# Kernel optimization log

Hardware: AMD Instinct MI355X
Metric: run time of the kernel (lower is better)

## Reference

```python
import jax, jax.numpy as jnp
import numpy as np

B, N, D = 2, 2048, 512
H, VD = 8, 64  # v_dim = hid_dim / n_head


def setup_inputs() -> dict:
    key = jax.random.key(0)
    k1, k2, k3, k4 = jax.random.split(key, 4)
    inputs = jax.random.normal(k1, (B, N, D), dtype=jnp.float32)
    # lecun_normal: std = 1/sqrt(fan_in) with fan_in = D
    s = 1.0 / np.sqrt(D)
    q_w = jax.random.normal(k2, (H, D, VD), dtype=jnp.float32) * s
    k_w = jax.random.normal(k3, (H, D, VD), dtype=jnp.float32) * s
    v_w = jax.random.normal(k4, (H, D, VD), dtype=jnp.float32) * s
    return {"inputs": inputs, "q_w": q_w, "k_w": k_w, "v_w": v_w}


def reference(inputs, q_w, k_w, v_w):
    # QKV projections: [B,N,D] x [H,D,VD] -> [B,H,N,VD]
    q = jnp.einsum('bnj,hjk->bhnk', inputs, q_w)
    k = jnp.einsum('bnj,hjk->bhnk', inputs, k_w)
    v = jnp.einsum('bnj,hjk->bhnk', inputs, v_w)
    scale = 1.0 / jnp.sqrt(jnp.asarray(VD, dtype=q.dtype))
    scores = jnp.einsum('bhik,bhjk->bhij', q, k) * scale  # [B,H,N,N]
    att = jax.nn.softmax(scores, axis=-1)
    out = jnp.einsum('bhnj,bhjd->bhnd', att, v)  # [B,H,N,VD]
    out = jnp.transpose(out, (0, 2, 1, 3)).reshape(inputs.shape[0], -1, H * VD)  # [B,N,hid_dim]
    # keras GELU default is exact (non-approximate)
    return jax.nn.gelu(out, approximate=False)
```

## Files before the change

kernel.cpp:

```cpp
#include <hip/hip_runtime.h>
#include <hip/hip_bf16.h>
#include <math.h>

#define BB 2
#define NN 2048
#define DD 512
#define HH 8
#define VD 64

typedef _Float16 half8 __attribute__((ext_vector_type(8)));
typedef _Float16 half4 __attribute__((ext_vector_type(4)));
typedef __fp16 fp16x2 __attribute__((ext_vector_type(2)));
typedef float f32x4 __attribute__((ext_vector_type(4)));

#define GLDS16(gp, lp) __builtin_amdgcn_global_load_lds( \
    (const __attribute__((address_space(1))) void*)(gp), \
    (__attribute__((address_space(3))) void*)(lp), 16, 0, 0)

__device__ __forceinline__ float fexp2(float x) {
#if __has_builtin(__builtin_amdgcn_exp2f)
    return __builtin_amdgcn_exp2f(x);
#else
    return exp2f(x);
#endif
}

__device__ __forceinline__ void stage8(const _Float16* gsrc, size_t ldg, int r0,
                                       _Float16* lbase, int lane) {
    int r8 = lane >> 3;
    int ce = ((lane & 7) ^ r8) << 3;
    const _Float16* g = gsrc + (size_t)(r0 + r8) * ldg + ce;
    GLDS16(g, lbase);
}

__device__ __forceinline__ half8 frag_ld(const _Float16* tile, int row, int cb) {
    int off = row * 128 + (cb ^ ((row & 7) << 4));
    return *(const half8*)((const char*)tile + off);
}

__device__ __forceinline__ float gelu_exact(float v) {
    return 0.5f * v * (1.f + erff(v * 0.70710678118654752f));
}

__global__ __launch_bounds__(256) void prep_kernel(
    const float* __restrict__ x,
    const float* __restrict__ qw, const float* __restrict__ kw,
    const float* __restrict__ vw,
    _Float16* __restrict__ wt, _Float16* __restrict__ xh)
{
    __shared__ float ls[64][65];
    const int t = threadIdx.x;
    const int bid = blockIdx.x;
    if (bid < 192) {
        const int kc = bid & 7, h = (bid >> 3) & 7, ty = bid >> 6;
        const float* src = (ty == 0) ? qw : (ty == 1) ? kw : vw;
#pragma unroll
        for (int j = 0; j < 4; ++j) {
            int idx = t + 256 * j;
            int k = idx >> 4, o4 = idx & 15;
            float4 v = *(const float4*)(src + ((size_t)(h * DD + kc * 64 + k) * VD + o4 * 4));
            ls[k][o4 * 4 + 0] = v.x; ls[k][o4 * 4 + 1] = v.y;
            ls[k][o4 * 4 + 2] = v.z; ls[k][o4 * 4 + 3] = v.w;
        }
        __syncthreads();
#pragma unroll
        for (int j = 0; j < 4; ++j) {
            int idx = t + 256 * j;
            int o = idx >> 4, k4 = idx & 15;
            half4 hv;
#pragma unroll
            for (int i = 0; i < 4; ++i) hv[i] = (_Float16)ls[k4 * 4 + i][o];
            *(half4*)(wt + ((size_t)(ty * HH + h) * VD + o) * DD + kc * 64 + k4 * 4) = hv;
        }
    } else {
        size_t idx = ((size_t)(bid - 192) * 256 + t) * 8;
        float4 a = *(const float4*)(x + idx);
        float4 b = *(const float4*)(x + idx + 4);
        half8 hv;
        hv[0] = (_Float16)a.x; hv[1] = (_Float16)a.y;
        hv[2] = (_Float16)a.z; hv[3] = (_Float16)a.w;
        hv[4] = (_Float16)b.x; hv[5] = (_Float16)b.y;
        hv[6] = (_Float16)b.z; hv[7] = (_Float16)b.w;
        *(half8*)(xh + idx) = hv;
    }
}

__global__ __launch_bounds__(256) void qkv_proj_kernel(
    const _Float16* __restrict__ xh,
    const _Float16* __restrict__ wt,
    _Float16* __restrict__ qsp,
    _Float16* __restrict__ kbp,
    _Float16* __restrict__ vtp)
{
    __shared__ __align__(16) _Float16 xls[2][4096];
    __shared__ __align__(16) _Float16 wls[2][12288];
    const int t = threadIdx.x;
    const int wave = t >> 6, lane = t & 63;
    const int lq = lane & 15, g = lane >> 4;
    const int bid = blockIdx.x;
    const int h = bid & 7;
    const int m0 = (bid >> 3) * 64;
    const int rbase = 32 * (wave >> 1);
    const int cbase = 96 * (wave & 1);

    f32x4 acc[2][6];
#pragma unroll
    for (int a = 0; a < 2; ++a)
#pragma unroll
        for (int c = 0; c < 6; ++c) acc[a][c] = (f32x4){0.f, 0.f, 0.f, 0.f};

    auto stage = [&](int buf, int ks) {
#pragma unroll
        for (int j = 0; j < 2; ++j) {
            int i = wave * 2 + j;
            stage8(xh + (size_t)m0 * DD + ks * 64, DD, i * 8, &xls[buf][i * 512], lane);
        }
#pragma unroll
        for (int j = 0; j < 6; ++j) {
            int i = wave * 6 + j;
            int ty = i >> 3;
            int ol = (i & 7) * 8;
            stage8(wt + ((size_t)(ty * HH + h) * VD + ol) * DD + ks * 64, DD, 0,
                   &wls[buf][i * 512], lane);
        }
    };

    stage(0, 0);
    stage(1, 1);
    for (int ks = 0; ks < 8; ++ks) {
        const int buf = ks & 1;
        if (ks < 7) asm volatile("s_waitcnt vmcnt(8)" ::: "memory");
        else        asm volatile("s_waitcnt vmcnt(0)" ::: "memory");
        __builtin_amdgcn_s_barrier();
        half8 af[2][2];
        half8 bf[6][2];
#pragma unroll
        for (int amt = 0; amt < 2; ++amt) {
            af[amt][0] = frag_ld(xls[buf], rbase + amt * 16 + lq, 16 * g);
            af[amt][1] = frag_ld(xls[buf], rbase + amt * 16 + lq, 64 + 16 * g);
        }
#pragma unroll
        for (int ct = 0; ct < 6; ++ct) {
            int wr = cbase + ct * 16 + lq;
            bf[ct][0] = frag_ld(wls[buf], wr, 16 * g);
            bf[ct][1] = frag_ld(wls[buf], wr, 64 + 16 * g);
        }
        asm volatile("s_waitcnt lgkmcnt(0)" ::: "memory");
        __builtin_amdgcn_sched_barrier(0);
        __builtin_amdgcn_s_barrier();
        if (ks + 2 < 8) stage(buf, ks + 2);
        __builtin_amdgcn_s_setprio(1);
#pragma unroll
        for (int ct = 0; ct < 6; ++ct) {
#pragma unroll
            for (int amt = 0; amt < 2; ++amt) {
                acc[amt][ct] = __builtin_amdgcn_mfma_f32_16x16x32_f16(af[amt][0], bf[ct][0], acc[amt][ct], 0, 0, 0);
                acc[amt][ct] = __builtin_amdgcn_mfma_f32_16x16x32_f16(af[amt][1], bf[ct][1], acc[amt][ct], 0, 0, 0);
            }
        }
        __builtin_amdgcn_s_setprio(0);
    }

#pragma unroll
    for (int ct = 0; ct < 6; ++ct) {
        int gcol = cbase + ct * 16 + lq;
        int ty = gcol >> 6, o = gcol & 63;
#pragma unroll
        for (int amt = 0; amt < 2; ++amt) {
#pragma unroll
            for (int i = 0; i < 4; ++i) {
                int ng = m0 + rbase + amt * 16 + 4 * g + i;
                int b = ng >> 11, nb = ng & (NN - 1);
                size_t bh = (size_t)(b * HH + h);
                float v = acc[amt][ct][i];
                if (ty == 0)      qsp[(bh * NN + nb) * VD + o] = (_Float16)(v * 0.18033688011112042f);
                else if (ty == 1) kbp[(bh * NN + nb) * VD + o] = (_Float16)v;
                else              vtp[(bh * VD + o) * NN + nb] = (_Float16)v;
            }
        }
    }
}

__global__ __launch_bounds__(256) void attn_kernel(
    const _Float16* __restrict__ qs,
    const _Float16* __restrict__ kb,
    const _Float16* __restrict__ vt,
    float* __restrict__ out)
{
    constexpr int NITER = NN / 64;
    __shared__ __align__(16) _Float16 kls[3][4096];
    __shared__ __align__(16) _Float16 vls[3][4096];
    const int t = threadIdx.x;
    const int wave = t >> 6, lane = t & 63;
    const int lq = lane & 15, g = lane >> 4;
    const int bid = blockIdx.x;
    const int xcd = bid & 7;
    const int bh = xcd * 2 + ((bid >> 3) & 1);
    const int qt = bid >> 4;
    const int qbase = qt * 64 + wave * 16;

    half8 qf[2];
    {
        const _Float16* qp = qs + ((size_t)bh * NN + qbase + lq) * VD + 8 * g;
        qf[0] = *(const half8*)qp;
        qf[1] = *(const half8*)(qp + 32);
    }

    const int r8 = lane >> 3;
    const int dchunk = (lane & 7) ^ r8;
    const int krow0 = 16 * (r8 >> 2) + 4 * wave + (r8 & 3);
    const _Float16* kgA = kb + (size_t)bh * NN * VD + (size_t)krow0 * VD + dchunk * 8;
    const int kvst = 16 * (dchunk & 3) + 8 * (dchunk >> 2);
    const _Float16* vgA = vt + (size_t)bh * VD * NN + (size_t)(wave * 16 + r8) * NN + kvst;

    f32x4 oacc[4];
#pragma unroll
    for (int mt = 0; mt < 4; ++mt) oacc[mt] = (f32x4){0.f, 0.f, 0.f, 0.f};
    float lsum = 0.f;

    auto stagekv = [&](_Float16* kd, _Float16* vd, int itn) {
        const _Float16* kp = kgA + (size_t)itn * (64 * VD);
        GLDS16(kp,           kd + wave * 1024);
        GLDS16(kp + 32 * VD, kd + wave * 1024 + 512);
        const _Float16* vp = vgA + itn * 64;
        GLDS16(vp,           vd + wave * 1024);
        GLDS16(vp + 8 * NN,  vd + wave * 1024 + 512);
    };

    _Float16 *k0 = &kls[0][0], *k1 = &kls[1][0], *k2 = &kls[2][0];
    _Float16 *v0 = &vls[0][0], *v1 = &vls[1][0], *v2 = &vls[2][0];
    stagekv(k0, v0, 0);
    stagekv(k1, v1, 1);
    stagekv(k2, v2, 2);

    union PU { fp16x2 h2[4]; half8 h8; };

    for (int j = 0; j < NITER; ++j) {
        if (j < NITER - 2)       asm volatile("s_waitcnt vmcnt(8)" ::: "memory");
        else if (j == NITER - 2) asm volatile("s_waitcnt vmcnt(4)" ::: "memory");
        else                     asm volatile("s_waitcnt vmcnt(0)" ::: "memory");
        __builtin_amdgcn_s_barrier();
        half8 kf[4][2], vf[2][4];
#pragma unroll
        for (int mt = 0; mt < 4; ++mt) {
            kf[mt][0] = frag_ld(k0, mt * 16 + lq, 16 * g);
            kf[mt][1] = frag_ld(k0, mt * 16 + lq, 64 + 16 * g);
        }
#pragma unroll
        for (int kc = 0; kc < 2; ++kc)
#pragma unroll
            for (int mt = 0; mt < 4; ++mt)
                vf[kc][mt] = frag_ld(v0, mt * 16 + lq, kc * 64 + 16 * g);
        asm volatile("s_waitcnt lgkmcnt(0)" ::: "memory");
        __builtin_amdgcn_sched_barrier(0);
        __builtin_amdgcn_s_barrier();
        if (j + 3 < NITER) stagekv(k0, v0, j + 3);
        f32x4 sv[4];
        __builtin_amdgcn_s_setprio(1);
#pragma unroll
        for (int mt = 0; mt < 4; ++mt) {
            sv[mt] = (f32x4){0.f, 0.f, 0.f, 0.f};
            sv[mt] = __builtin_amdgcn_mfma_f32_16x16x32_f16(kf[mt][0], qf[0], sv[mt], 0, 0, 0);
            sv[mt] = __builtin_amdgcn_mfma_f32_16x16x32_f16(kf[mt][1], qf[1], sv[mt], 0, 0, 0);
        }
        __builtin_amdgcn_s_setprio(0);
        PU pu[2];
#pragma unroll
        for (int mt = 0; mt < 4; ++mt) {
            float p0 = fexp2(sv[mt][0]);
            float p1 = fexp2(sv[mt][1]);
            float p2 = fexp2(sv[mt][2]);
            float p3 = fexp2(sv[mt][3]);
            lsum += (p0 + p1) + (p2 + p3);
            pu[mt >> 1].h2[(mt & 1) * 2 + 0] = __builtin_amdgcn_cvt_pkrtz(p0, p1);
            pu[mt >> 1].h2[(mt & 1) * 2 + 1] = __builtin_amdgcn_cvt_pkrtz(p2, p3);
        }
        __builtin_amdgcn_s_setprio(1);
#pragma unroll
        for (int kc = 0; kc < 2; ++kc)
#pragma unroll
            for (int mt = 0; mt < 4; ++mt)
                oacc[mt] = __builtin_amdgcn_mfma_f32_16x16x32_f16(vf[kc][mt], pu[kc].h8, oacc[mt], 0, 0, 0);
        __builtin_amdgcn_s_setprio(0);
        _Float16* tk = k0; k0 = k1; k1 = k2; k2 = tk;
        _Float16* tv = v0; v0 = v1; v1 = v2; v2 = tv;
    }

    const int b = bh >> 3, h = bh & 7;
    float l = lsum;
    l += __shfl_xor(l, 16, 64);
    l += __shfl_xor(l, 32, 64);
    float inv = 1.f / l;
    float* op = out + ((size_t)b * NN + qbase + lq) * (HH * VD) + h * VD;
#pragma unroll
    for (int mt = 0; mt < 4; ++mt) {
        float4 r;
        r.x = gelu_exact(oacc[mt][0] * inv);
        r.y = gelu_exact(oacc[mt][1] * inv);
        r.z = gelu_exact(oacc[mt][2] * inv);
        r.w = gelu_exact(oacc[mt][3] * inv);
        *(float4*)(op + mt * 16 + 4 * g) = r;
    }
}

extern "C" void kernel_launch(void* const* d_in, const int* in_sizes, int n_in,
                              void* d_out, int out_size, void* d_ws, size_t ws_size,
                              hipStream_t stream)
{
    const float* x  = (const float*)d_in[0];
    const float* qw = (const float*)d_in[1];
    const float* kw = (const float*)d_in[2];
    const float* vw = (const float*)d_in[3];
    float* out = (float*)d_out;

    _Float16* wt  = (_Float16*)d_ws;
    _Float16* xhp = wt  + 786432;
    _Float16* qsp = xhp + 2097152;
    _Float16* kbp = qsp + 2097152;
    _Float16* vtp = kbp + 2097152;

    hipLaunchKernelGGL(prep_kernel, dim3(192 + 1024), dim3(256), 0, stream,
                       x, qw, kw, vw, wt, xhp);
    hipLaunchKernelGGL(qkv_proj_kernel, dim3(512), dim3(256), 0, stream,
                       xhp, wt, qsp, kbp, vtp);
    hipLaunchKernelGGL(attn_kernel, dim3(512), dim3(256), 0, stream,
                       qsp, kbp, vtp, out);
}
```

Before: 52.97 us.

## Split KV across waves with shared Q tile and LDS reduction of partial outputs

The attention kernel switches from each wave owning 16 queries over all keys to each wave owning all 64 queries of the block but only a quarter of every 128-key chunk. The K/V tile doubles to 128 keys with double buffering, and partial outputs and row sums are reduced across waves through LDS at the end. V is stored in a permuted key order so that the P fragment layout matches the V fragments, and the LDS layout is widened and swizzled. This halves the number of loop iterations and barriers and raises MFMA work per LDS fragment load. In exchange it needs more accumulator registers (launch bounds now target 2 blocks) and adds a final cross-wave reduction.

```diff
diff --git a/kernel.cpp b/kernel.cpp
--- a/kernel.cpp
+++ b/kernel.cpp
@@ -35,6 +35,11 @@
 
 __device__ __forceinline__ half8 frag_ld(const _Float16* tile, int row, int cb) {
     int off = row * 128 + (cb ^ ((row & 7) << 4));
+    return *(const half8*)((const char*)tile + off);
+}
+
+__device__ __forceinline__ half8 frag_ldv(const _Float16* tile, int row, int cb) {
+    int off = row * 256 + (cb ^ ((row & 15) << 4));
     return *(const half8*)((const char*)tile + off);
 }
 
@@ -175,21 +180,23 @@
                 float v = acc[amt][ct][i];
                 if (ty == 0)      qsp[(bh * NN + nb) * VD + o] = (_Float16)(v * 0.18033688011112042f);
                 else if (ty == 1) kbp[(bh * NN + nb) * VD + o] = (_Float16)v;
-                else              vtp[(bh * VD + o) * NN + nb] = (_Float16)v;
+                else {
+                    int nbp = (nb & ~31) | (((nb >> 2) & 3) << 3) | (((nb >> 4) & 1) << 2) | (nb & 3);
+                    vtp[(bh * VD + o) * NN + nbp] = (_Float16)v;
+                }
             }
         }
     }
 }
 
-__global__ __launch_bounds__(256) void attn_kernel(
+__global__ __launch_bounds__(256, 2) void attn_kernel(
     const _Float16* __restrict__ qs,
     const _Float16* __restrict__ kb,
     const _Float16* __restrict__ vt,
     float* __restrict__ out)
 {
-    constexpr int NITER = NN / 64;
-    __shared__ __align__(16) _Float16 kls[3][4096];
-    __shared__ __align__(16) _Float16 vls[3][4096];
+    constexpr int NITER = NN / 128;
+    __shared__ __align__(16) char SM[65536 + 1024];
     const int t = threadIdx.x;
     const int wave = t >> 6, lane = t & 63;
     const int lq = lane & 15, g = lane >> 4;
@@ -197,109 +204,148 @@
     const int xcd = bid & 7;
     const int bh = xcd * 2 + ((bid >> 3) & 1);
     const int qt = bid >> 4;
-    const int qbase = qt * 64 + wave * 16;
-
-    half8 qf[2];
-    {
-        const _Float16* qp = qs + ((size_t)bh * NN + qbase + lq) * VD + 8 * g;
-        qf[0] = *(const half8*)qp;
-        qf[1] = *(const half8*)(qp + 32);
-    }
+    const int qbase = qt * 64;
+
+    half8 qf[4][2];
+#pragma unroll
+    for (int qg = 0; qg < 4; ++qg)
+#pragma unroll
+        for (int ds = 0; ds < 2; ++ds)
+            qf[qg][ds] = *(const half8*)(qs + ((size_t)bh * NN + qbase + 16 * qg + lq) * VD + 32 * ds + 8 * g);
 
     const int r8 = lane >> 3;
-    const int dchunk = (lane & 7) ^ r8;
-    const int krow0 = 16 * (r8 >> 2) + 4 * wave + (r8 & 3);
-    const _Float16* kgA = kb + (size_t)bh * NN * VD + (size_t)krow0 * VD + dchunk * 8;
-    const int kvst = 16 * (dchunk & 3) + 8 * (dchunk >> 2);
-    const _Float16* vgA = vt + (size_t)bh * VD * NN + (size_t)(wave * 16 + r8) * NN + kvst;
-
-    f32x4 oacc[4];
-#pragma unroll
-    for (int mt = 0; mt < 4; ++mt) oacc[mt] = (f32x4){0.f, 0.f, 0.f, 0.f};
-    float lsum = 0.f;
-
-    auto stagekv = [&](_Float16* kd, _Float16* vd, int itn) {
-        const _Float16* kp = kgA + (size_t)itn * (64 * VD);
-        GLDS16(kp,           kd + wave * 1024);
-        GLDS16(kp + 32 * VD, kd + wave * 1024 + 512);
-        const _Float16* vp = vgA + itn * 64;
-        GLDS16(vp,           vd + wave * 1024);
-        GLDS16(vp + 8 * NN,  vd + wave * 1024 + 512);
+    const _Float16* kS = kb + ((size_t)bh * NN + 32 * wave + r8) * VD + 8 * ((lane & 7) ^ r8);
+    const _Float16* vS[4];
+#pragma unroll
+    for (int uu = 0; uu < 4; ++uu) {
+        int vrow = 16 * wave + 4 * uu + g;
+        vS[uu] = vt + ((size_t)bh * VD + vrow) * NN + 8 * (lq ^ (vrow & 15));
+    }
+
+    _Float16* kb0 = (_Float16*)(SM);
+    _Float16* vb0 = (_Float16*)(SM + 16384);
+    _Float16* kb1 = (_Float16*)(SM + 32768);
+    _Float16* vb1 = (_Float16*)(SM + 49152);
+
+    auto stage = [&](int b, int j) {
+        _Float16* kd = (b ? kb1 : kb0) + 4 * wave * 512;
+        const _Float16* kp = kS + (size_t)j * 128 * VD;
+#pragma unroll
+        for (int uu = 0; uu < 4; ++uu)
+            GLDS16(kp + uu * 8 * VD, kd + uu * 512);
+        _Float16* vd = (b ? vb1 : vb0) + 4 * wave * 512;
+#pragma unroll
+        for (int uu = 0; uu < 4; ++uu)
+            GLDS16(vS[uu] + j * 128, vd + uu * 512);
     };
 
-    _Float16 *k0 = &kls[0][0], *k1 = &kls[1][0], *k2 = &kls[2][0];
-    _Float16 *v0 = &vls[0][0], *v1 = &vls[1][0], *v2 = &vls[2][0];
-    stagekv(k0, v0, 0);
-    stagekv(k1, v1, 1);
-    stagekv(k2, v2, 2);
+    f32x4 oacc[4][4];
+#pragma unroll
+    for (int qg = 0; qg < 4; ++qg)
+#pragma unroll
+        for (int dt = 0; dt < 4; ++dt) oacc[qg][dt] = (f32x4){0.f, 0.f, 0.f, 0.f};
+    float lsum[4] = {0.f, 0.f, 0.f, 0.f};
+
+    stage(0, 0);
+    stage(1, 1);
 
     union PU { fp16x2 h2[4]; half8 h8; };
 
     for (int j = 0; j < NITER; ++j) {
-        if (j < NITER - 2)       asm volatile("s_waitcnt vmcnt(8)" ::: "memory");
-        else if (j == NITER - 2) asm volatile("s_waitcnt vmcnt(4)" ::: "memory");
-        else                     asm volatile("s_waitcnt vmcnt(0)" ::: "memory");
+        const int b = j & 1;
+        if (j < NITER - 1) asm volatile("s_waitcnt vmcnt(8)" ::: "memory");
+        else               asm volatile("s_waitcnt vmcnt(0)" ::: "memory");
         __builtin_amdgcn_s_barrier();
-        half8 kf[4][2], vf[2][4];
-#pragma unroll
-        for (int mt = 0; mt < 4; ++mt) {
-            kf[mt][0] = frag_ld(k0, mt * 16 + lq, 16 * g);
-            kf[mt][1] = frag_ld(k0, mt * 16 + lq, 64 + 16 * g);
-        }
-#pragma unroll
-        for (int kc = 0; kc < 2; ++kc)
-#pragma unroll
-            for (int mt = 0; mt < 4; ++mt)
-                vf[kc][mt] = frag_ld(v0, mt * 16 + lq, kc * 64 + 16 * g);
+        const _Float16* kB = b ? kb1 : kb0;
+        const _Float16* vB = b ? vb1 : vb0;
+        half8 kf[2][2], vf[4];
+#pragma unroll
+        for (int mt = 0; mt < 2; ++mt)
+#pragma unroll
+            for (int ds = 0; ds < 2; ++ds)
+                kf[mt][ds] = frag_ld(kB, 32 * wave + 16 * mt + lq, 64 * ds + 16 * g);
+#pragma unroll
+        for (int dt = 0; dt < 4; ++dt)
+            vf[dt] = frag_ldv(vB, 16 * dt + lq, 64 * wave + 16 * g);
         asm volatile("s_waitcnt lgkmcnt(0)" ::: "memory");
         __builtin_amdgcn_sched_barrier(0);
         __builtin_amdgcn_s_barrier();
-        if (j + 3 < NITER) stagekv(k0, v0, j + 3);
-        f32x4 sv[4];
+        if (j + 2 < NITER) stage(b, j + 2);
+        f32x4 sacc[4][2];
         __builtin_amdgcn_s_setprio(1);
 #pragma unroll
-        for (int mt = 0; mt < 4; ++mt) {
-            sv[mt] = (f32x4){0.f, 0.f, 0.f, 0.f};
-            sv[mt] = __builtin_amdgcn_mfma_f32_16x16x32_f16(kf[mt][0], qf[0], sv[mt], 0, 0, 0);
-            sv[mt] = __builtin_amdgcn_mfma_f32_16x16x32_f16(kf[mt][1], qf[1], sv[mt], 0, 0, 0);
+        for (int qg = 0; qg < 4; ++qg) {
+#pragma unroll
+            for (int mt = 0; mt < 2; ++mt) {
+                f32x4 sv = (f32x4){0.f, 0.f, 0.f, 0.f};
+                sv = __builtin_amdgcn_mfma_f32_16x16x32_f16(kf[mt][0], qf[qg][0], sv, 0, 0, 0);
+                sv = __builtin_amdgcn_mfma_f32_16x16x32_f16(kf[mt][1], qf[qg][1], sv, 0, 0, 0);
+                sacc[qg][mt] = sv;
+            }
         }
         __builtin_amdgcn_s_setprio(0);
-        PU pu[2];
-#pragma unroll
-        for (int mt = 0; mt < 4; ++mt) {
-            float p0 = fexp2(sv[mt][0]);
-            float p1 = fexp2(sv[mt][1]);
-            float p2 = fexp2(sv[mt][2]);
-            float p3 = fexp2(sv[mt][3]);
-            lsum += (p0 + p1) + (p2 + p3);
-            pu[mt >> 1].h2[(mt & 1) * 2 + 0] = __builtin_amdgcn_cvt_pkrtz(p0, p1);
-            pu[mt >> 1].h2[(mt & 1) * 2 + 1] = __builtin_amdgcn_cvt_pkrtz(p2, p3);
+        PU pu[4];
+#pragma unroll
+        for (int qg = 0; qg < 4; ++qg) {
+            float p00 = fexp2(sacc[qg][0][0]);
+            float p01 = fexp2(sacc[qg][0][1]);
+            float p02 = fexp2(sacc[qg][0][2]);
+            float p03 = fexp2(sacc[qg][0][3]);
+            float p10 = fexp2(sacc[qg][1][0]);
+            float p11 = fexp2(sacc[qg][1][1]);
+            float p12 = fexp2(sacc[qg][1][2]);
+            float p13 = fexp2(sacc[qg][1][3]);
+            lsum[qg] += ((p00 + p01) + (p02 + p03)) + ((p10 + p11) + (p12 + p13));
+            pu[qg].h2[0] = __builtin_amdgcn_cvt_pkrtz(p00, p01);
+            pu[qg].h2[1] = __builtin_amdgcn_cvt_pkrtz(p02, p03);
+            pu[qg].h2[2] = __builtin_amdgcn_cvt_pkrtz(p10, p11);
+            pu[qg].h2[3] = __builtin_amdgcn_cvt_pkrtz(p12, p13);
         }
         __builtin_amdgcn_s_setprio(1);
 #pragma unroll
-        for (int kc = 0; kc < 2; ++kc)
-#pragma unroll
-            for (int mt = 0; mt < 4; ++mt)
-                oacc[mt] = __builtin_amdgcn_mfma_f32_16x16x32_f16(vf[kc][mt], pu[kc].h8, oacc[mt], 0, 0, 0);
+        for (int qg = 0; qg < 4; ++qg)
+#pragma unroll
+            for (int dt = 0; dt < 4; ++dt)
+                oacc[qg][dt] = __builtin_amdgcn_mfma_f32_16x16x32_f16(vf[dt], pu[qg].h8, oacc[qg][dt], 0, 0, 0);
         __builtin_amdgcn_s_setprio(0);
-        _Float16* tk = k0; k0 = k1; k1 = k2; k2 = tk;
-        _Float16* tv = v0; v0 = v1; v1 = v2; v2 = tv;
-    }
-
-    const int b = bh >> 3, h = bh & 7;
-    float l = lsum;
-    l += __shfl_xor(l, 16, 64);
-    l += __shfl_xor(l, 32, 64);
-    float inv = 1.f / l;
-    float* op = out + ((size_t)b * NN + qbase + lq) * (HH * VD) + h * VD;
-#pragma unroll
-    for (int mt = 0; mt < 4; ++mt) {
+    }
+
+#pragma unroll
+    for (int qg = 0; qg < 4; ++qg) {
+        lsum[qg] += __shfl_xor(lsum[qg], 16, 64);
+        lsum[qg] += __shfl_xor(lsum[qg], 32, 64);
+    }
+    float* lsm  = (float*)(SM + 65536);
+    float* sred = (float*)SM;
+    __syncthreads();
+    if (g == 0) {
+#pragma unroll
+        for (int qg = 0; qg < 4; ++qg) lsm[wave * 64 + 16 * qg + lq] = lsum[qg];
+    }
+#pragma unroll
+    for (int qg = 0; qg < 4; ++qg)
+#pragma unroll
+        for (int dt = 0; dt < 4; ++dt)
+            *(f32x4*)(sred + (size_t)wave * 4096 + (16 * qg + lq) * 64 + 16 * dt + 4 * g) = oacc[qg][dt];
+    __syncthreads();
+    const int b2 = bh >> 3, h = bh & 7;
+    const int q = t >> 2, cg = t & 3;
+    float lt = (lsm[q] + lsm[64 + q]) + (lsm[128 + q] + lsm[192 + q]);
+    float inv = 1.f / lt;
+    float* op = out + ((size_t)b2 * NN + qbase + q) * (HH * VD) + h * VD + 16 * cg;
+#pragma unroll
+    for (int c2 = 0; c2 < 4; ++c2) {
+        int off = q * 64 + 16 * cg + 4 * c2;
+        f32x4 o = *(const f32x4*)(sred + off);
+        o += *(const f32x4*)(sred + 4096 + off);
+        o += *(const f32x4*)(sred + 8192 + off);
+        o += *(const f32x4*)(sred + 12288 + off);
         float4 r;
-        r.x = gelu_exact(oacc[mt][0] * inv);
-        r.y = gelu_exact(oacc[mt][1] * inv);
-        r.z = gelu_exact(oacc[mt][2] * inv);
-        r.w = gelu_exact(oacc[mt][3] * inv);
-        *(float4*)(op + mt * 16 + 4 * g) = r;
+        r.x = gelu_exact(o[0] * inv);
+        r.y = gelu_exact(o[1] * inv);
+        r.z = gelu_exact(o[2] * inv);
+        r.w = gelu_exact(o[3] * inv);
+        *(float4*)(op + 4 * c2) = r;
     }
 }
 
```

New measurement: 53.21 us. About the same (+0.5%).
